# Kernel tuning notes

Hardware: AMD Instinct MI355X
Metric: run time of the kernel (lower is better)

Reference implementation:

```python
import jax, jax.numpy as jnp
import numpy as np

VOCAB, EMB, HID = 50257, 512, 1024
B, S = 64, 512

def setup_inputs() -> dict:
    key = jax.random.key(0)
    ks = jax.random.split(key, 10)
    sc = lambda fan_in: 1.0 / np.sqrt(fan_in)
    return {
        "x":   jax.random.randint(ks[0], (B, S), 0, VOCAB, dtype=jnp.int32),
        "emb": jax.random.normal(ks[1], (VOCAB, EMB), jnp.float32) * 0.02,
        "Wi1": jax.random.normal(ks[2], (EMB, HID), jnp.float32) * sc(EMB),
        "Wh1": jax.random.normal(ks[3], (HID, HID), jnp.float32) * sc(HID),
        "b1":  jnp.zeros((HID,), jnp.float32),
        "Wi2": jax.random.normal(ks[4], (HID, HID), jnp.float32) * sc(HID),
        "Wh2": jax.random.normal(ks[5], (HID, HID), jnp.float32) * sc(HID),
        "b2":  jnp.zeros((HID,), jnp.float32),
        "Wd":  jax.random.normal(ks[6], (HID, 1), jnp.float32) * sc(HID),
        "bd":  jnp.zeros((1,), jnp.float32),
    }

def reference(x, emb, Wi1, Wh1, b1, Wi2, Wh2, b2, Wd, bd):
    # Embed tokens: [B, S, EMB]
    xe = emb[x]
    batch = x.shape[0]
    hid = Wh1.shape[0]
    h0 = jnp.zeros((batch, hid), xe.dtype)

    # Fused two-layer Elman scan over time. SimpleCell: h' = tanh(x@Wi + b + h@Wh).
    # Dropout is deterministic at inference (train=False) -> identity.
    def step(carry, xt):
        h1, h2 = carry
        h1 = jnp.tanh(xt @ Wi1 + b1 + h1 @ Wh1)
        h2 = jnp.tanh(h1 @ Wi2 + b2 + h2 @ Wh2)
        return (h1, h2), None

    (_, h2_last), _ = jax.lax.scan(step, (h0, h0), jnp.swapaxes(xe, 0, 1))
    logits = h2_last @ Wd + bd  # [B, 1]
    return jax.nn.sigmoid(logits).squeeze(-1)
```

## Files before the change

### kernel.cpp

```cpp
#include <hip/hip_runtime.h>

#define B_   64
#define S_   512
#define EMB_ 512
#define HID_ 1024
#define NBLK_ 256

typedef float f32x4 __attribute__((ext_vector_type(4)));

__device__ __forceinline__ f32x4 ld_coh4(const float* p) {
    f32x4 d;
    asm volatile("global_load_dwordx4 %0, %1, off sc0 sc1" : "=v"(d) : "v"(p));
    return d;
}
__device__ __forceinline__ void st_coh4(float* p, f32x4 v) {
    asm volatile("global_store_dwordx4 %0, %1, off sc0 sc1" :: "v"(p), "v"(v) : "memory");
}
__device__ __forceinline__ void st_coh1u(unsigned* p, unsigned v) {
    asm volatile("global_store_dword %0, %1, off sc0 sc1" :: "v"(p), "v"(v) : "memory");
}
__device__ __forceinline__ unsigned ld_cohu_wait(const unsigned* p) {
    unsigned d;
    asm volatile("global_load_dword %0, %1, off sc0 sc1\n\t"
                 "s_waitcnt vmcnt(0)"
                 : "=v"(d) : "v"(p) : "memory");
    return d;
}

__global__ __launch_bounds__(256) void embed_gemm(
    const int* __restrict__ x, const float* __restrict__ emb,
    const float* __restrict__ Wi1, const float* __restrict__ b1,
    float* __restrict__ X1)
{
    __shared__ int   tok[128];
    __shared__ float aT[32][132];
    __shared__ float bl[32][68];

    const int tid = threadIdx.x;
    const int m0  = blockIdx.y * 128;
    const int n0  = blockIdx.x * 64;

    if (tid < 128) {
        int m = m0 + tid;
        tok[tid] = x[(m & 63) * S_ + (m >> 6)];
    }
    __syncthreads();

    const int tx = tid & 15;
    const int ty = tid >> 4;

    float acc[8][4];
#pragma unroll
    for (int r = 0; r < 8; ++r)
#pragma unroll
        for (int c = 0; c < 4; ++c) acc[r][c] = 0.f;

    for (int kt = 0; kt < EMB_; kt += 32) {
#pragma unroll
        for (int j = 0; j < 4; ++j) {
            int idx = tid + j * 256;
            int r   = idx >> 3;
            int k4  = (idx & 7) * 4;
            float4 v = *(const float4*)(emb + (size_t)tok[r] * EMB_ + kt + k4);
            aT[k4 + 0][r] = v.x; aT[k4 + 1][r] = v.y;
            aT[k4 + 2][r] = v.z; aT[k4 + 3][r] = v.w;
        }
#pragma unroll
        for (int j = 0; j < 2; ++j) {
            int idx = tid + j * 256;
            int k   = idx >> 4;
            int c4  = (idx & 15) * 4;
            *(float4*)&bl[k][c4] =
                *(const float4*)(Wi1 + (size_t)(kt + k) * HID_ + n0 + c4);
        }
        __syncthreads();

#pragma unroll 4
        for (int k = 0; k < 32; ++k) {
            float4 a0 = *(const float4*)&aT[k][ty * 8];
            float4 a1 = *(const float4*)&aT[k][ty * 8 + 4];
            float4 bv = *(const float4*)&bl[k][tx * 4];
            float ar[8] = {a0.x, a0.y, a0.z, a0.w, a1.x, a1.y, a1.z, a1.w};
            float bc[4] = {bv.x, bv.y, bv.z, bv.w};
#pragma unroll
            for (int r = 0; r < 8; ++r)
#pragma unroll
                for (int c = 0; c < 4; ++c) acc[r][c] += ar[r] * bc[c];
        }
        __syncthreads();
    }

    float4 bias = *(const float4*)(b1 + n0 + tx * 4);
#pragma unroll
    for (int r = 0; r < 8; ++r) {
        int m = m0 + ty * 8 + r;
        float4 o;
        o.x = acc[r][0] + bias.x; o.y = acc[r][1] + bias.y;
        o.z = acc[r][2] + bias.z; o.w = acc[r][3] + bias.w;
        *(float4*)(X1 + (size_t)m * HID_ + n0 + tx * 4) = o;
    }
}

__device__ __forceinline__ f32x4 shfl_xor4(f32x4 v, int m) {
    f32x4 r;
#pragma unroll
    for (int e = 0; e < 4; ++e) r[e] = __shfl_xor(v[e], m, 64);
    return r;
}

__global__ __launch_bounds__(256, 1) void rnn_scan(
    const float* __restrict__ X1, const float* __restrict__ Wh1,
    const float* __restrict__ Wi2, const float* __restrict__ Wh2,
    const float* __restrict__ b2, float* __restrict__ hb,
    float* __restrict__ p1, float* __restrict__ p2,
    unsigned int* __restrict__ flagsA, unsigned int* __restrict__ flagsB)
{
    __shared__ float w1s[128 * 32];
    __shared__ float w2s[128 * 32];
    __shared__ float w3s[128 * 32];

    const int tid = threadIdx.x;
    const int bk  = blockIdx.x;
    const int kg  = bk >> 5;
    const int cg  = bk & 31;
    const int cgp = bk >> 3;
    const int k0  = kg * 128;
    const int cs0 = cg * 32;

    for (int idx = tid; idx < 1024; idx += 256) {
        int k  = idx >> 3, c4 = (idx & 7) * 4;
        int sc = c4 ^ (((k >> 5) & 3) << 3);
        *(f32x4*)&w1s[k * 32 + sc] = *(const f32x4*)(Wh1 + (size_t)(k0 + k) * HID_ + cs0 + c4);
        *(f32x4*)&w2s[k * 32 + sc] = *(const f32x4*)(Wi2 + (size_t)(k0 + k) * HID_ + cs0 + c4);
        *(f32x4*)&w3s[k * 32 + sc] = *(const f32x4*)(Wh2 + (size_t)(k0 + k) * HID_ + cs0 + c4);
    }

    const int row = tid >> 2;
    const int kq  = tid & 3;
    const int kqs = kq << 3;
    const int kb0 = kq & 1;
    const int kb1 = (kq >> 1) & 1;

    const f32x4 b2v = *(const f32x4*)(b2 + bk * 4);

    float* h1buf[2] = { hb, hb + 65536 };
    float* h2buf[2] = { hb + 131072, hb + 196608 };

    __syncthreads();

    for (int i = 0; i <= S_; ++i) {
        if (i >= 1) {
            const unsigned* fb = flagsB + (size_t)(i - 1) * 256;
            if (tid < 40) {
                int idx = (tid < 32) ? (kg * 32 + tid) : (cg * 8 + (tid - 32));
                while (ld_cohu_wait(fb + idx) == 0) __builtin_amdgcn_s_sleep(1);
            }
            __syncthreads();
        }

        const float* h1src = h1buf[(i + 1) & 1] + row * HID_ + k0 + kq * 32;
        const float* h2src = h2buf[i & 1]       + row * HID_ + k0 + kq * 32;

        f32x4 va[8], vb[8];
#pragma unroll
        for (int c = 0; c < 8; ++c) {
            va[c] = ld_coh4(h1src + c * 4);
            vb[c] = ld_coh4(h2src + c * 4);
        }

        f32x4 a1[8], a2[8];
#pragma unroll
        for (int cc = 0; cc < 8; ++cc) { a1[cc] = (f32x4){0,0,0,0}; a2[cc] = (f32x4){0,0,0,0}; }

#pragma unroll
        for (int c = 0; c < 8; ++c) {
            asm volatile("s_waitcnt vmcnt(%0)" :: "i"(14 - 2 * c) : "memory");
            __builtin_amdgcn_sched_barrier(0);
#pragma unroll
            for (int j = 0; j < 4; ++j) {
                const int k = kq * 32 + c * 4 + j;
                const float hx = va[c][j];
                const float hy = vb[c][j];
                const float* w1r = &w1s[k * 32];
                const float* w2r = &w2s[k * 32];
                const float* w3r = &w3s[k * 32];
#pragma unroll
                for (int cc = 0; cc < 8; ++cc) {
                    const int sc = (cc * 4) ^ kqs;
                    f32x4 wv1 = *(const f32x4*)(w1r + sc);
                    f32x4 wv2 = *(const f32x4*)(w2r + sc);
                    f32x4 wv3 = *(const f32x4*)(w3r + sc);
                    a1[cc] += hx * wv1;
                    a2[cc] += hx * wv2 + hy * wv3;
                }
            }
        }

        f32x4 r1[4], r2[4];
#pragma unroll
        for (int t = 0; t < 4; ++t) {
            const int ik = (t >> 1) * 4 + (t & 1);
            f32x4 keep1 = kb0 ? a1[ik + 2] : a1[ik];
            f32x4 send1 = kb0 ? a1[ik]     : a1[ik + 2];
            f32x4 keep2 = kb0 ? a2[ik + 2] : a2[ik];
            f32x4 send2 = kb0 ? a2[ik]     : a2[ik + 2];
            r1[t] = keep1 + shfl_xor4(send1, 1);
            r2[t] = keep2 + shfl_xor4(send2, 1);
        }
        f32x4 f1a, f1b, f2a, f2b;
        {
            f32x4 k1a = kb1 ? r1[2] : r1[0];
            f32x4 s1a = kb1 ? r1[0] : r1[2];
            f32x4 k1b = kb1 ? r1[3] : r1[1];
            f32x4 s1b = kb1 ? r1[1] : r1[3];
            f32x4 k2a = kb1 ? r2[2] : r2[0];
            f32x4 s2a = kb1 ? r2[0] : r2[2];
            f32x4 k2b = kb1 ? r2[3] : r2[1];
            f32x4 s2b = kb1 ? r2[1] : r2[3];
            f1a = k1a + shfl_xor4(s1a, 2);
            f1b = k1b + shfl_xor4(s1b, 2);
            f2a = k2a + shfl_xor4(s2a, 2);
            f2b = k2b + shfl_xor4(s2b, 2);
        }

        {
            float* pp1 = p1 + ((size_t)kg * 64 + row) * HID_ + cs0 + kq * 8;
            float* pp2 = p2 + ((size_t)kg * 64 + row) * HID_ + cs0 + kq * 8;
            st_coh4(pp1,     f1a);
            st_coh4(pp1 + 4, f1b);
            st_coh4(pp2,     f2a);
            st_coh4(pp2 + 4, f2b);
        }

        asm volatile("s_waitcnt vmcnt(0)" ::: "memory");
        __syncthreads();
        if (tid == 0) st_coh1u(flagsA + (size_t)i * 256 + cg * 8 + kg, 1u);

        {
            const unsigned* fa = flagsA + (size_t)i * 256 + cgp * 8;
            if (tid < 8) {
                while (ld_cohu_wait(fa + tid) == 0) __builtin_amdgcn_s_sleep(1);
            }
            __syncthreads();
        }

        {
            const float* q1 = p1 + ((size_t)(2 * kq) * 64 + row) * HID_ + bk * 4;
            const float* q2 = p2 + ((size_t)(2 * kq) * 64 + row) * HID_ + bk * 4;
            f32x4 pa = ld_coh4(q1);
            f32x4 pb = ld_coh4(q1 + (size_t)64 * HID_);
            f32x4 pc = ld_coh4(q2);
            f32x4 pd = ld_coh4(q2 + (size_t)64 * HID_);

            f32x4 xv = (f32x4){0,0,0,0};
            if (i < S_)
                xv = *(const f32x4*)(X1 + ((size_t)i * B_ + row) * HID_ + bk * 4);

            asm volatile("s_waitcnt vmcnt(0)" ::: "memory");
            __builtin_amdgcn_sched_barrier(0);

            f32x4 s1 = pa + pb;
            f32x4 s2 = pc + pd;
#pragma unroll
            for (int m = 1; m <= 2; m <<= 1) {
                s1 += shfl_xor4(s1, m);
                s2 += shfl_xor4(s2, m);
            }

            if (kq == 0) {
                if (i < S_) {
                    f32x4 o;
                    o[0] = tanhf(xv[0] + s1[0]); o[1] = tanhf(xv[1] + s1[1]);
                    o[2] = tanhf(xv[2] + s1[2]); o[3] = tanhf(xv[3] + s1[3]);
                    st_coh4(h1buf[i & 1] + row * HID_ + bk * 4, o);
                }
                if (i >= 1) {
                    f32x4 o;
                    o[0] = tanhf(s2[0] + b2v[0]); o[1] = tanhf(s2[1] + b2v[1]);
                    o[2] = tanhf(s2[2] + b2v[2]); o[3] = tanhf(s2[3] + b2v[3]);
                    st_coh4(h2buf[(i + 1) & 1] + row * HID_ + bk * 4, o);
                }
            }
        }

        if (i < S_) {
            asm volatile("s_waitcnt vmcnt(0)" ::: "memory");
            __syncthreads();
            if (tid == 0) st_coh1u(flagsB + (size_t)i * 256 + bk, 1u);
        }
    }
}

__global__ void dense_sigmoid(const float* __restrict__ h2,
                              const float* __restrict__ Wd,
                              const float* __restrict__ bd,
                              float* __restrict__ out)
{
    int b = blockIdx.x, lane = threadIdx.x;
    float s = 0.f;
    for (int j = lane; j < HID_; j += 64) s += h2[b * HID_ + j] * Wd[j];
#pragma unroll
    for (int off = 32; off > 0; off >>= 1) s += __shfl_down(s, off, 64);
    if (lane == 0) out[b] = 1.f / (1.f + expf(-(s + bd[0])));
}

extern "C" void kernel_launch(void* const* d_in, const int* in_sizes, int n_in,
                              void* d_out, int out_size, void* d_ws, size_t ws_size,
                              hipStream_t stream)
{
    const int*   x   = (const int*)  d_in[0];
    const float* emb = (const float*)d_in[1];
    const float* Wi1 = (const float*)d_in[2];
    const float* Wh1 = (const float*)d_in[3];
    const float* b1  = (const float*)d_in[4];
    const float* Wi2 = (const float*)d_in[5];
    const float* Wh2 = (const float*)d_in[6];
    const float* b2  = (const float*)d_in[7];
    const float* Wd  = (const float*)d_in[8];
    const float* bd  = (const float*)d_in[9];
    float* out = (float*)d_out;

    char* w = (char*)d_ws;
    float*        hb     = (float*)w;
    unsigned int* flagsA = (unsigned int*)(w + 1048576);
    unsigned int* flagsB = (unsigned int*)(w + 1573888);
    float*        p1     = (float*)(w + 2098176);
    float*        p2     = (float*)(w + 4195328);
    float*        X1     = (float*)(w + 6292480);

    hipMemsetAsync(w, 0, 2098176, stream);

    dim3 gA(HID_ / 64, (S_ * B_) / 128);
    embed_gemm<<<gA, dim3(256), 0, stream>>>(x, emb, Wi1, b1, X1);

    const float* X1c = X1;
    void* args[] = { (void*)&X1c, (void*)&Wh1, (void*)&Wi2, (void*)&Wh2,
                     (void*)&b2, (void*)&hb, (void*)&p1, (void*)&p2,
                     (void*)&flagsA, (void*)&flagsB };
    hipLaunchCooperativeKernel((const void*)rnn_scan, dim3(NBLK_), dim3(256),
                               args, 0, stream);

    dense_sigmoid<<<64, 64, 0, stream>>>(hb + 196608, Wd, bd, out);
}
```

Before: 14.10 ms.

## Split batch rows across two block groups to shrink per-step sync fan-in

Repartitions the persistent RNN scan so each block handles 32 batch rows with a 128x64 weight slice instead of all 64 rows with a 128x32 slice. The two row groups synchronize independently, so each block waits on fewer flags and the second-stage reduction uses an 8-way shuffle over k-slices instead of a 4-way one. The h-vector loads are now double-buffered in 16-element chunks. The risks are losing the LDS bank swizzle, which may cause bank conflicts on the wider rows, and more redundant h reads per block.

```diff
diff --git a/kernel.cpp b/kernel.cpp
--- a/kernel.cpp
+++ b/kernel.cpp
@@ -6,7 +6,8 @@
 #define HID_ 1024
 #define NBLK_ 256
 
-typedef float f32x4 __attribute__((ext_vector_type(4)));
+typedef float    f32x4 __attribute__((ext_vector_type(4)));
+typedef unsigned u32x4 __attribute__((ext_vector_type(4)));
 
 __device__ __forceinline__ f32x4 ld_coh4(const float* p) {
     f32x4 d;
@@ -115,33 +116,34 @@
     float* __restrict__ p1, float* __restrict__ p2,
     unsigned int* __restrict__ flagsA, unsigned int* __restrict__ flagsB)
 {
-    __shared__ float w1s[128 * 32];
-    __shared__ float w2s[128 * 32];
-    __shared__ float w3s[128 * 32];
+    __shared__ float w1s[128 * 64];
+    __shared__ float w2s[128 * 64];
+    __shared__ float w3s[128 * 64];
 
     const int tid = threadIdx.x;
     const int bk  = blockIdx.x;
-    const int kg  = bk >> 5;
-    const int cg  = bk & 31;
-    const int cgp = bk >> 3;
+    const int rg  = bk >> 7;
+    const int kg  = (bk >> 4) & 7;
+    const int cg  = bk & 15;
+    const int jj  = bk & 127;
     const int k0  = kg * 128;
-    const int cs0 = cg * 32;
-
-    for (int idx = tid; idx < 1024; idx += 256) {
-        int k  = idx >> 3, c4 = (idx & 7) * 4;
-        int sc = c4 ^ (((k >> 5) & 3) << 3);
-        *(f32x4*)&w1s[k * 32 + sc] = *(const f32x4*)(Wh1 + (size_t)(k0 + k) * HID_ + cs0 + c4);
-        *(f32x4*)&w2s[k * 32 + sc] = *(const f32x4*)(Wi2 + (size_t)(k0 + k) * HID_ + cs0 + c4);
-        *(f32x4*)&w3s[k * 32 + sc] = *(const f32x4*)(Wh2 + (size_t)(k0 + k) * HID_ + cs0 + c4);
-    }
-
-    const int row = tid >> 2;
-    const int kq  = tid & 3;
-    const int kqs = kq << 3;
-    const int kb0 = kq & 1;
-    const int kb1 = (kq >> 1) & 1;
-
-    const f32x4 b2v = *(const f32x4*)(b2 + bk * 4);
+    const int cs0 = cg * 64;
+    const int r0  = rg * 32;
+
+    for (int idx = tid; idx < 2048; idx += 256) {
+        int k = idx >> 4, c4 = (idx & 15) * 4;
+        *(f32x4*)&w1s[k * 64 + c4] = *(const f32x4*)(Wh1 + (size_t)(k0 + k) * HID_ + cs0 + c4);
+        *(f32x4*)&w2s[k * 64 + c4] = *(const f32x4*)(Wi2 + (size_t)(k0 + k) * HID_ + cs0 + c4);
+        *(f32x4*)&w3s[k * 64 + c4] = *(const f32x4*)(Wh2 + (size_t)(k0 + k) * HID_ + cs0 + c4);
+    }
+
+    const int row32 = tid >> 3;
+    const int c8    = tid & 7;
+    const int row32b = tid >> 3;
+    const int kq8    = tid & 7;
+
+    const f32x4 b2va = *(const f32x4*)(b2 + jj * 8);
+    const f32x4 b2vb = *(const f32x4*)(b2 + jj * 8 + 4);
 
     float* h1buf[2] = { hb, hb + 65536 };
     float* h2buf[2] = { hb + 131072, hb + 196608 };
@@ -150,135 +152,143 @@
 
     for (int i = 0; i <= S_; ++i) {
         if (i >= 1) {
-            const unsigned* fb = flagsB + (size_t)(i - 1) * 256;
-            if (tid < 40) {
-                int idx = (tid < 32) ? (kg * 32 + tid) : (cg * 8 + (tid - 32));
+            const unsigned* fb = flagsB + (size_t)(i - 1) * 256 + rg * 128;
+            if (tid < 24) {
+                int idx = (tid < 16) ? (kg * 16 + tid) : (cg * 8 + (tid - 16));
                 while (ld_cohu_wait(fb + idx) == 0) __builtin_amdgcn_s_sleep(1);
             }
             __syncthreads();
         }
 
-        const float* h1src = h1buf[(i + 1) & 1] + row * HID_ + k0 + kq * 32;
-        const float* h2src = h2buf[i & 1]       + row * HID_ + k0 + kq * 32;
-
-        f32x4 va[8], vb[8];
-#pragma unroll
-        for (int c = 0; c < 8; ++c) {
-            va[c] = ld_coh4(h1src + c * 4);
-            vb[c] = ld_coh4(h2src + c * 4);
-        }
-
-        f32x4 a1[8], a2[8];
-#pragma unroll
-        for (int cc = 0; cc < 8; ++cc) { a1[cc] = (f32x4){0,0,0,0}; a2[cc] = (f32x4){0,0,0,0}; }
-
-#pragma unroll
-        for (int c = 0; c < 8; ++c) {
-            asm volatile("s_waitcnt vmcnt(%0)" :: "i"(14 - 2 * c) : "memory");
+        const float* h1src = h1buf[(i + 1) & 1] + (r0 + row32) * HID_ + k0;
+        const float* h2src = h2buf[i & 1]       + (r0 + row32) * HID_ + k0;
+
+        f32x4 a1lo = {0,0,0,0}, a1hi = {0,0,0,0};
+        f32x4 a2lo = {0,0,0,0}, a2hi = {0,0,0,0};
+
+        f32x4 A1[4], A2[4], B1[4], B2[4];
+
+#pragma unroll
+        for (int r = 0; r < 4; ++r) {
+            A1[r] = ld_coh4(h1src + r * 4);
+            A2[r] = ld_coh4(h2src + r * 4);
+        }
+
+#pragma unroll
+        for (int it = 0; it < 8; ++it) {
+            if (it < 7) {
+                const int kn = (it + 1) * 16;
+                if (it & 1) {
+#pragma unroll
+                    for (int r = 0; r < 4; ++r) {
+                        A1[r] = ld_coh4(h1src + kn + r * 4);
+                        A2[r] = ld_coh4(h2src + kn + r * 4);
+                    }
+                } else {
+#pragma unroll
+                    for (int r = 0; r < 4; ++r) {
+                        B1[r] = ld_coh4(h1src + kn + r * 4);
+                        B2[r] = ld_coh4(h2src + kn + r * 4);
+                    }
+                }
+            }
+            if (it < 7) asm volatile("s_waitcnt vmcnt(8)" ::: "memory");
+            else        asm volatile("s_waitcnt vmcnt(0)" ::: "memory");
             __builtin_amdgcn_sched_barrier(0);
-#pragma unroll
-            for (int j = 0; j < 4; ++j) {
-                const int k = kq * 32 + c * 4 + j;
-                const float hx = va[c][j];
-                const float hy = vb[c][j];
-                const float* w1r = &w1s[k * 32];
-                const float* w2r = &w2s[k * 32];
-                const float* w3r = &w3s[k * 32];
-#pragma unroll
-                for (int cc = 0; cc < 8; ++cc) {
-                    const int sc = (cc * 4) ^ kqs;
-                    f32x4 wv1 = *(const f32x4*)(w1r + sc);
-                    f32x4 wv2 = *(const f32x4*)(w2r + sc);
-                    f32x4 wv3 = *(const f32x4*)(w3r + sc);
-                    a1[cc] += hx * wv1;
-                    a2[cc] += hx * wv2 + hy * wv3;
+
+            const f32x4* c1 = (it & 1) ? B1 : A1;
+            const f32x4* c2 = (it & 1) ? B2 : A2;
+
+#pragma unroll
+            for (int q = 0; q < 4; ++q) {
+#pragma unroll
+                for (int e = 0; e < 4; ++e) {
+                    const int kk = it * 16 + q * 4 + e;
+                    const float hx = c1[q][e];
+                    const float hy = c2[q][e];
+                    const float* w1r = &w1s[kk * 64 + c8 * 8];
+                    const float* w2r = &w2s[kk * 64 + c8 * 8];
+                    const float* w3r = &w3s[kk * 64 + c8 * 8];
+                    f32x4 wv1a = *(const f32x4*)(w1r);
+                    f32x4 wv1b = *(const f32x4*)(w1r + 4);
+                    f32x4 wv2a = *(const f32x4*)(w2r);
+                    f32x4 wv2b = *(const f32x4*)(w2r + 4);
+                    f32x4 wv3a = *(const f32x4*)(w3r);
+                    f32x4 wv3b = *(const f32x4*)(w3r + 4);
+                    a1lo += hx * wv1a;  a1hi += hx * wv1b;
+                    a2lo += hx * wv2a + hy * wv3a;
+                    a2hi += hx * wv2b + hy * wv3b;
                 }
             }
         }
 
-        f32x4 r1[4], r2[4];
-#pragma unroll
-        for (int t = 0; t < 4; ++t) {
-            const int ik = (t >> 1) * 4 + (t & 1);
-            f32x4 keep1 = kb0 ? a1[ik + 2] : a1[ik];
-            f32x4 send1 = kb0 ? a1[ik]     : a1[ik + 2];
-            f32x4 keep2 = kb0 ? a2[ik + 2] : a2[ik];
-            f32x4 send2 = kb0 ? a2[ik]     : a2[ik + 2];
-            r1[t] = keep1 + shfl_xor4(send1, 1);
-            r2[t] = keep2 + shfl_xor4(send2, 1);
-        }
-        f32x4 f1a, f1b, f2a, f2b;
         {
-            f32x4 k1a = kb1 ? r1[2] : r1[0];
-            f32x4 s1a = kb1 ? r1[0] : r1[2];
-            f32x4 k1b = kb1 ? r1[3] : r1[1];
-            f32x4 s1b = kb1 ? r1[1] : r1[3];
-            f32x4 k2a = kb1 ? r2[2] : r2[0];
-            f32x4 s2a = kb1 ? r2[0] : r2[2];
-            f32x4 k2b = kb1 ? r2[3] : r2[1];
-            f32x4 s2b = kb1 ? r2[1] : r2[3];
-            f1a = k1a + shfl_xor4(s1a, 2);
-            f1b = k1b + shfl_xor4(s1b, 2);
-            f2a = k2a + shfl_xor4(s2a, 2);
-            f2b = k2b + shfl_xor4(s2b, 2);
-        }
-
-        {
-            float* pp1 = p1 + ((size_t)kg * 64 + row) * HID_ + cs0 + kq * 8;
-            float* pp2 = p2 + ((size_t)kg * 64 + row) * HID_ + cs0 + kq * 8;
-            st_coh4(pp1,     f1a);
-            st_coh4(pp1 + 4, f1b);
-            st_coh4(pp2,     f2a);
-            st_coh4(pp2 + 4, f2b);
+            float* pp1 = p1 + ((size_t)kg * 64 + r0 + row32) * HID_ + cs0 + c8 * 8;
+            float* pp2 = p2 + ((size_t)kg * 64 + r0 + row32) * HID_ + cs0 + c8 * 8;
+            st_coh4(pp1,     a1lo); st_coh4(pp1 + 4, a1hi);
+            st_coh4(pp2,     a2lo); st_coh4(pp2 + 4, a2hi);
         }
 
         asm volatile("s_waitcnt vmcnt(0)" ::: "memory");
         __syncthreads();
-        if (tid == 0) st_coh1u(flagsA + (size_t)i * 256 + cg * 8 + kg, 1u);
+        if (tid == 0) st_coh1u(flagsA + (size_t)i * 256 + bk, 1u);
 
         {
-            const unsigned* fa = flagsA + (size_t)i * 256 + cgp * 8;
+            const unsigned* fa = flagsA + (size_t)i * 256 + rg * 128;
             if (tid < 8) {
-                while (ld_cohu_wait(fa + tid) == 0) __builtin_amdgcn_s_sleep(1);
+                while (ld_cohu_wait(fa + tid * 16 + (jj >> 3)) == 0)
+                    __builtin_amdgcn_s_sleep(1);
             }
             __syncthreads();
         }
 
         {
-            const float* q1 = p1 + ((size_t)(2 * kq) * 64 + row) * HID_ + bk * 4;
-            const float* q2 = p2 + ((size_t)(2 * kq) * 64 + row) * HID_ + bk * 4;
-            f32x4 pa = ld_coh4(q1);
-            f32x4 pb = ld_coh4(q1 + (size_t)64 * HID_);
-            f32x4 pc = ld_coh4(q2);
-            f32x4 pd = ld_coh4(q2 + (size_t)64 * HID_);
-
-            f32x4 xv = (f32x4){0,0,0,0};
-            if (i < S_)
-                xv = *(const f32x4*)(X1 + ((size_t)i * B_ + row) * HID_ + bk * 4);
+            const float* q1 = p1 + ((size_t)kq8 * 64 + r0 + row32b) * HID_ + jj * 8;
+            const float* q2 = p2 + ((size_t)kq8 * 64 + r0 + row32b) * HID_ + jj * 8;
+            f32x4 s1a = ld_coh4(q1);
+            f32x4 s1b = ld_coh4(q1 + 4);
+            f32x4 s2a = ld_coh4(q2);
+            f32x4 s2b = ld_coh4(q2 + 4);
+
+            f32x4 xva = {0,0,0,0}, xvb = {0,0,0,0};
+            if (i < S_) {
+                const float* xp = X1 + ((size_t)i * B_ + r0 + row32b) * HID_ + jj * 8;
+                xva = *(const f32x4*)(xp);
+                xvb = *(const f32x4*)(xp + 4);
+            }
 
             asm volatile("s_waitcnt vmcnt(0)" ::: "memory");
             __builtin_amdgcn_sched_barrier(0);
 
-            f32x4 s1 = pa + pb;
-            f32x4 s2 = pc + pd;
-#pragma unroll
-            for (int m = 1; m <= 2; m <<= 1) {
-                s1 += shfl_xor4(s1, m);
-                s2 += shfl_xor4(s2, m);
-            }
-
-            if (kq == 0) {
+#pragma unroll
+            for (int m = 1; m <= 4; m <<= 1) {
+                s1a += shfl_xor4(s1a, m);
+                s1b += shfl_xor4(s1b, m);
+                s2a += shfl_xor4(s2a, m);
+                s2b += shfl_xor4(s2b, m);
+            }
+
+            if (kq8 == 0) {
+                const int row = r0 + row32b;
                 if (i < S_) {
-                    f32x4 o;
-                    o[0] = tanhf(xv[0] + s1[0]); o[1] = tanhf(xv[1] + s1[1]);
-                    o[2] = tanhf(xv[2] + s1[2]); o[3] = tanhf(xv[3] + s1[3]);
-                    st_coh4(h1buf[i & 1] + row * HID_ + bk * 4, o);
+                    f32x4 oa, ob;
+#pragma unroll
+                    for (int e = 0; e < 4; ++e) {
+                        oa[e] = tanhf(xva[e] + s1a[e]);
+                        ob[e] = tanhf(xvb[e] + s1b[e]);
+                    }
+                    float* hp = h1buf[i & 1] + row * HID_ + jj * 8;
+                    st_coh4(hp, oa); st_coh4(hp + 4, ob);
                 }
                 if (i >= 1) {
-                    f32x4 o;
-                    o[0] = tanhf(s2[0] + b2v[0]); o[1] = tanhf(s2[1] + b2v[1]);
-                    o[2] = tanhf(s2[2] + b2v[2]); o[3] = tanhf(s2[3] + b2v[3]);
-                    st_coh4(h2buf[(i + 1) & 1] + row * HID_ + bk * 4, o);
+                    f32x4 oa, ob;
+#pragma unroll
+                    for (int e = 0; e < 4; ++e) {
+                        oa[e] = tanhf(s2a[e] + b2va[e]);
+                        ob[e] = tanhf(s2b[e] + b2vb[e]);
+                    }
+                    float* hp = h2buf[(i + 1) & 1] + row * HID_ + jj * 8;
+                    st_coh4(hp, oa); st_coh4(hp + 4, ob);
                 }
             }
         }
```

New measurement: 11.98 ms. -15.0%, faster.
